# Performance work log

Hardware: AMD Instinct MI355X
Metric: run time of the kernel (lower is better)

Reference implementation:

```python
import jax, jax.numpy as jnp
import numpy as np
from jax import lax

B, C_IN, C_OUT, N, R, K = 16, 64, 64, 32768, 32, 3
GROUPS, GN_EPS = 8, 1e-5


def swish(x):
    return x * jax.nn.sigmoid(x)


def group_norm(x, gamma, beta):
    b, c = x.shape[:2]
    xg = x.reshape(b, GROUPS, -1)
    mu = xg.mean(-1, keepdims=True)
    var = xg.var(-1, keepdims=True)
    xn = ((xg - mu) * lax.rsqrt(var + GN_EPS)).reshape(x.shape)
    shp = (1, c) + (1,) * (x.ndim - 2)
    return xn * gamma.reshape(shp) + beta.reshape(shp)


def conv3d(x, w, b):
    y = lax.conv_general_dilated(x, w, (1, 1, 1), 'SAME',
                                 dimension_numbers=('NCDHW', 'OIDHW', 'NCDHW'))
    return y + b.reshape(1, -1, 1, 1, 1)


def voxelize(features, coords):
    # features [B,C,N], coords [B,3,N] -> vox [B,C,R,R,R], norm_coords [B,3,N] in [0,R-1]
    c = coords - coords.mean(axis=2, keepdims=True)
    scale = jnp.linalg.norm(c, axis=1, keepdims=True).max(axis=2, keepdims=True) * 2.0  # eps=0
    norm = jnp.clip((c / scale + 0.5) * R, 0.0, R - 1)
    vc = jnp.round(norm).astype(jnp.int32)
    idx = (vc[:, 0] * R + vc[:, 1]) * R + vc[:, 2]  # [B,N] flat voxel index

    def per_batch(f, i):  # f [C,N], i [N] -> [C, R^3] scatter-average
        sums = jax.ops.segment_sum(f.T, i, num_segments=R ** 3)  # [R^3, C]
        cnt = jax.ops.segment_sum(jnp.ones(i.shape, f.dtype), i, num_segments=R ** 3)
        return (sums / jnp.maximum(cnt, 1.0)[:, None]).T

    vox = jax.vmap(per_batch)(features, idx).reshape(features.shape[0], features.shape[1], R, R, R)
    return vox, norm


def trilinear_devoxelize(vox, coords):
    # vox [B,C,R,R,R], coords [B,3,N] float in [0,R-1] -> [B,C,N]
    b, c = vox.shape[:2]
    flat = vox.reshape(b, c, R ** 3)
    c0f = jnp.floor(coords)
    f = coords - c0f
    i0 = jnp.clip(c0f.astype(jnp.int32), 0, R - 1)
    i1 = jnp.clip(i0 + 1, 0, R - 1)
    out = jnp.zeros((b, c, coords.shape[2]), vox.dtype)
    for xi, wx in ((i0[:, 0], 1.0 - f[:, 0]), (i1[:, 0], f[:, 0])):
        for yi, wy in ((i0[:, 1], 1.0 - f[:, 1]), (i1[:, 1], f[:, 1])):
            for zi, wz in ((i0[:, 2], 1.0 - f[:, 2]), (i1[:, 2], f[:, 2])):
                idx = (xi * R + yi) * R + zi  # [B,N]
                w = (wx * wy * wz)[:, None, :]
                out = out + jnp.take_along_axis(flat, idx[:, None, :], axis=2) * w
    return out


def setup_inputs():
    key = jax.random.key(0)
    ks = jax.random.split(key, 6)
    s1 = 1.0 / np.sqrt(C_IN * K ** 3)
    s2 = 1.0 / np.sqrt(C_OUT * K ** 3)
    sp = 1.0 / np.sqrt(C_IN)
    return {
        'features': jax.random.normal(ks[0], (B, C_IN, N), jnp.float32),
        'coords': jax.random.normal(ks[1], (B, 3, N), jnp.float32),
        'w1': jax.random.normal(ks[2], (C_OUT, C_IN, K, K, K), jnp.float32) * s1,
        'b1': jnp.zeros((C_OUT,), jnp.float32),
        'g1': jnp.ones((C_OUT,), jnp.float32),
        'be1': jnp.zeros((C_OUT,), jnp.float32),
        'w2': jax.random.normal(ks[3], (C_OUT, C_OUT, K, K, K), jnp.float32) * s2,
        'b2': jnp.zeros((C_OUT,), jnp.float32),
        'g2': jnp.ones((C_OUT,), jnp.float32),
        'be2': jnp.zeros((C_OUT,), jnp.float32),
        'wp': jax.random.normal(ks[4], (C_OUT, C_IN), jnp.float32) * sp,
        'bp': jnp.zeros((C_OUT,), jnp.float32),
        'gp': jnp.ones((C_OUT,), jnp.float32),
        'bep': jnp.zeros((C_OUT,), jnp.float32),
    }


def reference(features, coords, w1, b1, g1, be1, w2, b2, g2, be2, wp, bp, gp, bep):
    coords_sg = lax.stop_gradient(coords)  # torch: coords.detach() inside Voxelization
    vox, norm_coords = voxelize(features, coords_sg)
    h = swish(group_norm(conv3d(vox, w1, b1), g1, be1))
    # Dropout(0.1) is identity in eval mode
    h = swish(group_norm(conv3d(h, w2, b2), g2, be2))
    vpts = trilinear_devoxelize(h, norm_coords)
    pf = swish(group_norm(jnp.einsum('oc,bcn->bon', wp, features) + bp[None, :, None], gp, bep))
    return (vpts + pf, coords)
```

## Files before the change

kernel.cpp:

```cpp
#include <hip/hip_runtime.h>
#include <hip/hip_bf16.h>
#include <math.h>

#define BB   16
#define CCH  64
#define NPT  32768
#define RR   32
#define R3   32768
#define GSZ  262144
#define VOXB 2228224

typedef __attribute__((ext_vector_type(8))) short bfx8;
typedef __attribute__((ext_vector_type(8))) unsigned short usx8;
typedef __attribute__((ext_vector_type(16))) float f32x16;

__device__ __forceinline__ short f2bf(float f) {
    unsigned u = __builtin_bit_cast(unsigned, f);
    u += 0x7fff + ((u >> 16) & 1);
    return (short)(u >> 16);
}
__device__ __forceinline__ float bf2f(unsigned short s) {
    unsigned u = ((unsigned)s) << 16;
    return __builtin_bit_cast(float, u);
}

__device__ __forceinline__ float blockReduceSumF(float v) {
    __shared__ float sm[16];
    #pragma unroll
    for (int o = 32; o > 0; o >>= 1) v += __shfl_down(v, o);
    __syncthreads();
    if ((threadIdx.x & 63) == 0) sm[threadIdx.x >> 6] = v;
    __syncthreads();
    float s = 0.f;
    int nw = blockDim.x >> 6;
    for (int i = 0; i < nw; ++i) s += sm[i];
    return s;
}

__device__ __forceinline__ float blockReduceMaxF(float v) {
    __shared__ float sm[16];
    #pragma unroll
    for (int o = 32; o > 0; o >>= 1) v = fmaxf(v, __shfl_down(v, o));
    __syncthreads();
    if ((threadIdx.x & 63) == 0) sm[threadIdx.x >> 6] = v;
    __syncthreads();
    float s = sm[0];
    int nw = blockDim.x >> 6;
    for (int i = 1; i < nw; ++i) s = fmaxf(s, sm[i]);
    return s;
}

__global__ void k_cstat_sum(const float* __restrict__ coords, float* __restrict__ csum) {
    int b = blockIdx.x >> 3, seg = blockIdx.x & 7;
    const float* cb = coords + (size_t)b * 3 * NPT;
    int n0 = seg << 12;
    float sx = 0.f, sy = 0.f, sz = 0.f;
    for (int n = n0 + threadIdx.x; n < n0 + 4096; n += 256) {
        sx += cb[n]; sy += cb[NPT + n]; sz += cb[2 * NPT + n];
    }
    sx = blockReduceSumF(sx);
    sy = blockReduceSumF(sy);
    sz = blockReduceSumF(sz);
    if (threadIdx.x == 0) {
        atomicAdd(&csum[b * 4 + 0], sx);
        atomicAdd(&csum[b * 4 + 1], sy);
        atomicAdd(&csum[b * 4 + 2], sz);
    }
}

__global__ void k_cstat_max(const float* __restrict__ coords, const float* __restrict__ csum,
                            int* __restrict__ cmax) {
    int b = blockIdx.x >> 3, seg = blockIdx.x & 7;
    const float* cb = coords + (size_t)b * 3 * NPT;
    float mx = csum[b * 4 + 0] * (1.f / NPT);
    float my = csum[b * 4 + 1] * (1.f / NPT);
    float mz = csum[b * 4 + 2] * (1.f / NPT);
    int n0 = seg << 12;
    float mn = 0.f;
    for (int n = n0 + threadIdx.x; n < n0 + 4096; n += 256) {
        float x = cb[n] - mx, y = cb[NPT + n] - my, z = cb[2 * NPT + n] - mz;
        mn = fmaxf(mn, sqrtf(x * x + y * y + z * z));
    }
    mn = blockReduceMaxF(mn);
    if (threadIdx.x == 0) atomicMax(&cmax[b], __float_as_int(mn));
}

__global__ void k_norm_idx(const float* __restrict__ coords, const float* __restrict__ csum,
                           const int* __restrict__ cmax,
                           float* __restrict__ normc, int* __restrict__ vidx,
                           int* __restrict__ hist, float* __restrict__ out2) {
    int t = blockIdx.x * 256 + threadIdx.x;
    int b = t >> 15, n = t & 32767;
    float mx = csum[b * 4 + 0] * (1.f / NPT);
    float my = csum[b * 4 + 1] * (1.f / NPT);
    float mz = csum[b * 4 + 2] * (1.f / NPT);
    float scale = 2.f * __int_as_float(cmax[b]);
    const float* cb = coords + (size_t)b * 3 * NPT;
    float x = cb[n], y = cb[NPT + n], z = cb[2 * NPT + n];
    float nx = fminf(fmaxf(((x - mx) / scale + 0.5f) * 32.f, 0.f), 31.f);
    float ny = fminf(fmaxf(((y - my) / scale + 0.5f) * 32.f, 0.f), 31.f);
    float nz = fminf(fmaxf(((z - mz) / scale + 0.5f) * 32.f, 0.f), 31.f);
    float* nb = normc + (size_t)b * 3 * NPT;
    nb[n] = nx; nb[NPT + n] = ny; nb[2 * NPT + n] = nz;
    int vx = (int)rintf(nx), vy = (int)rintf(ny), vz = (int)rintf(nz);
    int v = (vx * 32 + vy) * 32 + vz;
    vidx[t] = v;
    atomicAdd(&hist[(b << 15) + v], 1);
    float* o2 = out2 + (size_t)b * 3 * NPT;
    o2[n] = x; o2[NPT + n] = y; o2[2 * NPT + n] = z;
}

__global__ __launch_bounds__(1024) void k_prefix(const int* __restrict__ hist,
                                                 int* __restrict__ startB,
                                                 int* __restrict__ base) {
    int b = blockIdx.x;
    int tid = threadIdx.x;
    const int* h = hist + (b << 15);
    int loc[32];
    int s = 0;
    #pragma unroll
    for (int j = 0; j < 32; ++j) { loc[j] = h[tid * 32 + j]; s += loc[j]; }
    __shared__ int sm[1024];
    sm[tid] = s;
    __syncthreads();
    for (int o = 1; o < 1024; o <<= 1) {
        int v = (tid >= o) ? sm[tid - o] : 0;
        __syncthreads();
        sm[tid] += v;
        __syncthreads();
    }
    int run = (tid ? sm[tid - 1] : 0);
    #pragma unroll
    for (int j = 0; j < 32; ++j) {
        int idx = (b << 15) + tid * 32 + j;
        startB[idx] = run;
        base[idx] = run;
        run += loc[j];
    }
}

__global__ __launch_bounds__(256) void k_reorder(const float* __restrict__ feat,
                                                 const int* __restrict__ vidx,
                                                 int* __restrict__ base,
                                                 short* __restrict__ featT) {
    __shared__ float tile[64][65];
    __shared__ int sslot[64];
    int blk = blockIdx.x;
    int b = blk >> 9;
    int n0 = (blk & 511) << 6;
    int tid = threadIdx.x;
    const float* fb = feat + ((size_t)b << 21);
    for (int e = tid; e < 64 * 16; e += 256) {
        int c = e >> 4, n4 = e & 15;
        float4 v4 = *(const float4*)(fb + ((size_t)c << 15) + n0 + n4 * 4);
        tile[c][n4 * 4 + 0] = v4.x; tile[c][n4 * 4 + 1] = v4.y;
        tile[c][n4 * 4 + 2] = v4.z; tile[c][n4 * 4 + 3] = v4.w;
    }
    if (tid < 64) {
        int v = vidx[(b << 15) + n0 + tid];
        sslot[tid] = atomicAdd(&base[(b << 15) + v], 1);
    }
    __syncthreads();
    int p = tid >> 2, q = tid & 3;
    int slot = sslot[p];
    short* dst = featT + (((size_t)((b << 15) + slot)) << 6) + q * 16;
    unsigned pk[8];
    #pragma unroll
    for (int k = 0; k < 8; ++k) {
        unsigned lo16 = (unsigned short)f2bf(tile[q * 16 + 2 * k][p]);
        unsigned hi16 = (unsigned short)f2bf(tile[q * 16 + 2 * k + 1][p]);
        pk[k] = lo16 | (hi16 << 16);
    }
    *(int4*)dst = make_int4(pk[0], pk[1], pk[2], pk[3]);
    *(int4*)(dst + 8) = make_int4(pk[4], pk[5], pk[6], pk[7]);
}

__global__ void k_vox_accum(const short* __restrict__ featT, const int* __restrict__ startB,
                            const int* __restrict__ base, short* __restrict__ vout) {
    int t = blockIdx.x * 256 + threadIdx.x;
    int lane4 = t & 15;
    int v = (t >> 4) & 32767;
    int b = t >> 19;
    int start = startB[(b << 15) + v];
    int end   = base[(b << 15) + v];
    float4 acc = make_float4(0.f, 0.f, 0.f, 0.f);
    const short* fT = featT + (((size_t)b << 15) << 6) + lane4 * 4;
    for (int p = start; p < end; ++p) {
        short4 hv = *(const short4*)(fT + ((size_t)p << 6));
        acc.x += bf2f((unsigned short)hv.x);
        acc.y += bf2f((unsigned short)hv.y);
        acc.z += bf2f((unsigned short)hv.z);
        acc.w += bf2f((unsigned short)hv.w);
    }
    float rc = 1.f / fmaxf((float)(end - start), 1.f);
    short4 pk;
    pk.x = f2bf(acc.x * rc); pk.y = f2bf(acc.y * rc);
    pk.z = f2bf(acc.z * rc); pk.w = f2bf(acc.w * rc);
    *(short4*)(vout + (size_t)b * VOXB + ((size_t)(v >> 5) * 34 + (v & 31) + 1) * 64 + lane4 * 4) = pk;
}

__global__ void k_padzero(short* __restrict__ v) {
    int t = blockIdx.x * 256 + threadIdx.x;
    int q = t & 7, zp = (t >> 3) & 1, xy = (t >> 4) & 1023, b = t >> 14;
    int z = zp ? 33 : 0;
    *(int4*)(v + (size_t)b * VOXB + ((size_t)xy * 34 + z) * 64 + q * 8) = make_int4(0, 0, 0, 0);
}

__global__ void k_wprep(const float* __restrict__ w, short* __restrict__ wT) {
    int e = blockIdx.x * 256 + threadIdx.x;
    int ci = e & 63, co = (e >> 6) & 63, k = e >> 12;
    wT[e] = f2bf(w[(size_t)(co * 64 + ci) * 27 + k]);
}

template<bool FUSE>
__global__ __launch_bounds__(512, 4) void k_conv_mfma(
    const short* __restrict__ vin, const short* __restrict__ wT,
    const float* __restrict__ bias,
    const float* __restrict__ stin, const float* __restrict__ gin,
    const float* __restrict__ bein,
    short* __restrict__ vout, float* __restrict__ st)
{
    __shared__ short lds[36 * 1088];
    __shared__ float sred[8][2];
    int bid = blockIdx.x;
    int xcd = bid & 7, sub = bid >> 3;
    int b = (xcd << 1) | (sub >> 6);
    int tile = sub & 63;
    int x0 = (tile >> 3) << 2, y0 = (tile & 7) << 2;
    int tid = threadIdx.x;
    int wv8 = tid >> 6;
    int cb = wv8 & 1, xl = wv8 >> 1;
    int l = tid & 63, lo = l & 31, hi = l >> 5;
    const short* vb = vin + (size_t)b * VOXB;
    int xo = x0 + xl;
    if (tid < 16) ((float*)sred)[tid] = 0.f;

    f32x16 acc[4];
    #pragma unroll
    for (int j = 0; j < 4; ++j)
        #pragma unroll
        for (int i = 0; i < 16; ++i) acc[j][i] = 0.f;

    #pragma unroll
    for (int h = 0; h < 2; ++h) {
        if (h) __syncthreads();
        for (int e = tid; e < 4896; e += 512) {
            int line = e / 136, r = e - line * 136;
            int z = r >> 2, q = r & 3;
            int xx = line / 6, yy = line - xx * 6;
            int xi = x0 + xx - 1, yi = y0 + yy - 1;
            bool inb = ((unsigned)xi < 32u) && ((unsigned)yi < 32u);
            int4 v = make_int4(0, 0, 0, 0);
            if (inb)
                v = *(const int4*)(vb + ((size_t)(xi * 32 + yi) * 34 + z) * 64 + h * 32 + q * 8);
            if (FUSE) {
                if (inb && z >= 1 && z <= 32) {
                    int ci0 = h * 32 + q * 8, cg = ci0 >> 3;
                    float s = stin[((b << 3) + cg) * 2 + 0];
                    float s2 = stin[((b << 3) + cg) * 2 + 1];
                    float mean = s * (1.f / 262144.f);
                    float rstd = rsqrtf(s2 * (1.f / 262144.f) - mean * mean + 1e-5f);
                    float4 ga = *(const float4*)(gin + ci0);
                    float4 gb = *(const float4*)(gin + ci0 + 4);
                    float4 ba = *(const float4*)(bein + ci0);
                    float4 bb = *(const float4*)(bein + ci0 + 4);
                    float gm[8] = {ga.x, ga.y, ga.z, ga.w, gb.x, gb.y, gb.z, gb.w};
                    float bt[8] = {ba.x, ba.y, ba.z, ba.w, bb.x, bb.y, bb.z, bb.w};
                    unsigned short* hv = (unsigned short*)&v;
                    #pragma unroll
                    for (int i = 0; i < 8; ++i) {
                        float f = bf2f(hv[i]);
                        float g = (f - mean) * rstd * gm[i] + bt[i];
                        float sw = g / (1.f + __expf(-g));
                        hv[i] = (unsigned short)f2bf(sw);
                    }
                }
            }
            int dst = line * 1088 + z * 32 + ((q * 8) ^ ((z & 3) << 3));
            *(int4*)(lds + dst) = v;
        }
        __syncthreads();
        const short* wbase = wT + lo * 64 + h * 32 + hi * 8 + cb * 2048;
        #pragma unroll
        for (int dx = 0; dx < 3; ++dx) {
            const short* ldsx = lds + ((xl + dx) * 6) * 1088;
            #pragma unroll
            for (int dz = 0; dz < 3; ++dz) {
                int zz = lo + dz;
                int swz = (zz & 3) << 3;
                const short* bcol = ldsx + zz * 32;
                #pragma unroll
                for (int s = 0; s < 2; ++s) {
                    int slot = (s * 16 + hi * 8) ^ swz;
                    const short* wt0 = wbase + (dx * 9 + dz) * 4096 + s * 16;
                    bfx8 w0 = *(const bfx8*)(wt0);
                    bfx8 w1 = *(const bfx8*)(wt0 + 3 * 4096);
                    bfx8 w2 = *(const bfx8*)(wt0 + 6 * 4096);
                    #pragma unroll
                    for (int L = 0; L < 6; ++L) {
                        bfx8 bv = *(const bfx8*)(bcol + L * 1088 + slot);
                        if (L <= 3)
                            acc[L] = __builtin_amdgcn_mfma_f32_32x32x16_bf16(w0, bv, acc[L], 0, 0, 0);
                        if (L >= 1 && L <= 4)
                            acc[L-1] = __builtin_amdgcn_mfma_f32_32x32x16_bf16(w1, bv, acc[L-1], 0, 0, 0);
                        if (L >= 2)
                            acc[L-2] = __builtin_amdgcn_mfma_f32_32x32x16_bf16(w2, bv, acc[L-2], 0, 0, 0);
                    }
                }
            }
        }
    }

    float gs[4], gs2[4];
    #pragma unroll
    for (int g = 0; g < 4; ++g) { gs[g] = 0.f; gs2[g] = 0.f; }
    short* ob = vout + (size_t)b * VOXB;
    #pragma unroll
    for (int j = 0; j < 4; ++j) {
        size_t rb = ((size_t)(xo * 32 + y0 + j) * 34 + 1 + lo) * 64;
        #pragma unroll
        for (int q = 0; q < 4; ++q) {
            int co0 = cb * 32 + hi * 4 + q * 8;
            float v0 = acc[j][q * 4 + 0] + bias[co0 + 0];
            float v1 = acc[j][q * 4 + 1] + bias[co0 + 1];
            float v2 = acc[j][q * 4 + 2] + bias[co0 + 2];
            float v3 = acc[j][q * 4 + 3] + bias[co0 + 3];
            gs[q] += v0 + v1 + v2 + v3;
            gs2[q] += v0 * v0 + v1 * v1 + v2 * v2 + v3 * v3;
            short4 pk;
            pk.x = f2bf(v0); pk.y = f2bf(v1); pk.z = f2bf(v2); pk.w = f2bf(v3);
            *(short4*)(ob + rb + co0) = pk;
        }
    }
    #pragma unroll
    for (int q = 0; q < 4; ++q) {
        float s = gs[q], s2 = gs2[q];
        #pragma unroll
        for (int o = 32; o > 0; o >>= 1) { s += __shfl_down(s, o); s2 += __shfl_down(s2, o); }
        if (l == 0) { atomicAdd(&sred[cb * 4 + q][0], s); atomicAdd(&sred[cb * 4 + q][1], s2); }
    }
    __syncthreads();
    if (tid < 8) {
        atomicAdd(&st[((b << 3) + tid) * 2 + 0], sred[tid][0]);
        atomicAdd(&st[((b << 3) + tid) * 2 + 1], sred[tid][1]);
    }
}

__global__ void k_gn_apply_b(short* __restrict__ v, const float* __restrict__ st,
                             const float* __restrict__ gamma, const float* __restrict__ beta) {
    int e = blockIdx.x * 256 + threadIdx.x;
    int cg = e & 7, vx = (e >> 3) & 32767, b = e >> 18;
    float s = st[(b * 8 + cg) * 2 + 0], s2 = st[(b * 8 + cg) * 2 + 1];
    float mean = s * (1.f / 262144.f);
    float var = s2 * (1.f / 262144.f) - mean * mean;
    float rstd = rsqrtf(var + 1e-5f);
    short* p = v + (size_t)b * VOXB + ((size_t)(vx >> 5) * 34 + (vx & 31) + 1) * 64 + cg * 8;
    usx8 hv = *(const usx8*)p;
    usx8 ov;
    #pragma unroll
    for (int i = 0; i < 8; ++i) {
        int co = cg * 8 + i;
        float f = bf2f(hv[i]);
        float g = (f - mean) * rstd * gamma[co] + beta[co];
        float sw = g / (1.f + __expf(-g));
        ov[i] = (unsigned short)f2bf(sw);
    }
    *(usx8*)p = ov;
}

__global__ __launch_bounds__(256) void k_point(const float* __restrict__ feat,
                                               const float* __restrict__ wp,
                                               const float* __restrict__ bp,
                                               short* __restrict__ pbuf,
                                               float* __restrict__ stp) {
    __shared__ float s_f[64][64];
    __shared__ float s_w[64][68];
    __shared__ float sred[8][2];
    int nblk = blockIdx.x * 64;
    int b = blockIdx.y;
    int tid = threadIdx.x;
    if (tid < 16) ((float*)sred)[tid] = 0.f;
    const float* fb = feat + (((size_t)b * CCH) << 15);
    for (int e = tid; e < 64 * 64; e += 256) {
        int c = e >> 6, nn = e & 63;
        s_f[c][nn] = fb[(((size_t)c) << 15) + nblk + nn];
        s_w[nn][c] = wp[e];
    }
    __syncthreads();
    int o0 = (tid >> 4) << 2;
    int n0 = (tid & 15) << 2;
    float acc[4][4] = {{0.f}};
    for (int c = 0; c < 64; ++c) {
        float4 fv = *(const float4*)&s_f[c][n0];
        float4 wv = *(const float4*)&s_w[c][o0];
        float fvv[4] = {fv.x, fv.y, fv.z, fv.w};
        float wvv[4] = {wv.x, wv.y, wv.z, wv.w};
        #pragma unroll
        for (int j = 0; j < 4; ++j)
            #pragma unroll
            for (int i = 0; i < 4; ++i) acc[j][i] += wvv[j] * fvv[i];
    }
    float s = 0.f, s2 = 0.f;
    #pragma unroll
    for (int j = 0; j < 4; ++j) {
        float bb = bp[o0 + j];
        short* op = pbuf + (((size_t)(b * CCH + o0 + j)) << 15) + nblk + n0;
        short4 pk;
        float v0 = acc[j][0] + bb, v1 = acc[j][1] + bb;
        float v2 = acc[j][2] + bb, v3 = acc[j][3] + bb;
        s += v0 + v1 + v2 + v3;
        s2 += v0 * v0 + v1 * v1 + v2 * v2 + v3 * v3;
        pk.x = f2bf(v0); pk.y = f2bf(v1); pk.z = f2bf(v2); pk.w = f2bf(v3);
        *(short4*)op = pk;
    }
    int g = o0 >> 3;
    atomicAdd(&sred[g][0], s);
    atomicAdd(&sred[g][1], s2);
    __syncthreads();
    if (tid < 8) {
        atomicAdd(&stp[(b * 8 + tid) * 2 + 0], sred[tid][0]);
        atomicAdd(&stp[(b * 8 + tid) * 2 + 1], sred[tid][1]);
    }
}

__global__ void k_final(const short* __restrict__ h, const float* __restrict__ normc,
                        const float* __restrict__ stp, const float* __restrict__ gp,
                        const float* __restrict__ bep, const short* __restrict__ pbuf,
                        float* __restrict__ out1) {
    int tid = threadIdx.x;
    int s = tid & 7, pp = tid >> 3;
    int pt = blockIdx.x * 32 + pp;
    int b = pt >> 15, n = pt & 32767;
    const float* nb = normc + (size_t)b * 3 * NPT;
    float nx = nb[n], ny = nb[NPT + n], nz = nb[2 * NPT + n];
    float fxf = floorf(nx), fyf = floorf(ny), fzf = floorf(nz);
    float fx = nx - fxf, fy = ny - fyf, fz = nz - fzf;
    int x0 = (int)fxf; x0 = x0 < 31 ? x0 : 31;
    int y0 = (int)fyf; y0 = y0 < 31 ? y0 : 31;
    int z0 = (int)fzf; z0 = z0 < 31 ? z0 : 31;
    int x1 = x0 + 1 < 31 ? x0 + 1 : 31;
    int y1 = y0 + 1 < 31 ? y0 + 1 : 31;
    int z1 = z0 + 1 < 31 ? z0 + 1 : 31;
    float wx0 = 1.f - fx, wx1 = fx, wy0 = 1.f - fy, wy1 = fy, wz0 = 1.f - fz, wz1 = fz;
    const short* hb = h + (size_t)b * VOXB + s * 8;
    float acc[8];
    #pragma unroll
    for (int i = 0; i < 8; ++i) acc[i] = 0.f;
    #pragma unroll
    for (int cx = 0; cx < 2; ++cx) {
        int xi = cx ? x1 : x0; float wxx = cx ? wx1 : wx0;
        #pragma unroll
        for (int cy = 0; cy < 2; ++cy) {
            int yi = cy ? y1 : y0; float wyy = cy ? wy1 : wy0;
            #pragma unroll
            for (int cz = 0; cz < 2; ++cz) {
                int zi = cz ? z1 : z0; float wzz = cz ? wz1 : wz0;
                float w = wxx * wyy * wzz;
                usx8 hv = *(const usx8*)(hb + ((size_t)(xi * 32 + yi) * 34 + zi + 1) * 64);
                #pragma unroll
                for (int i = 0; i < 8; ++i) acc[i] = fmaf(w, bf2f(hv[i]), acc[i]);
            }
        }
    }
    float ss = stp[(b * 8 + s) * 2 + 0], ss2 = stp[(b * 8 + s) * 2 + 1];
    float mean = ss * (1.f / 262144.f);
    float rstd = rsqrtf(ss2 * (1.f / 262144.f) - mean * mean + 1e-5f);
    const short* pb = pbuf + (((size_t)(b * CCH)) << 15) + n;
    #pragma unroll
    for (int i = 0; i < 8; ++i) {
        int co = s * 8 + i;
        float* op = out1 + (((size_t)(b * CCH + co)) << 15) + n;
        float pv = bf2f((unsigned short)pb[((size_t)co) << 15]);
        float g = (pv - mean) * rstd * gp[co] + bep[co];
        float sw = g / (1.f + __expf(-g));
        *op = acc[i] + sw;
    }
}

extern "C" void kernel_launch(void* const* d_in, const int* in_sizes, int n_in,
                              void* d_out, int out_size, void* d_ws, size_t ws_size,
                              hipStream_t stream) {
    const float* feat   = (const float*)d_in[0];
    const float* coords = (const float*)d_in[1];
    const float* w1  = (const float*)d_in[2];
    const float* b1  = (const float*)d_in[3];
    const float* g1  = (const float*)d_in[4];
    const float* be1 = (const float*)d_in[5];
    const float* w2  = (const float*)d_in[6];
    const float* b2  = (const float*)d_in[7];
    const float* g2  = (const float*)d_in[8];
    const float* be2 = (const float*)d_in[9];
    const float* wp  = (const float*)d_in[10];
    const float* bp  = (const float*)d_in[11];
    const float* gp  = (const float*)d_in[12];
    const float* bep = (const float*)d_in[13];

    float* out1 = (float*)d_out;
    float* out2 = out1 + (size_t)BB * CCH * NPT;

    const size_t reg0Bytes = (size_t)BB * NPT * CCH * 4;
    short* featT    = (short*)d_ws;
    short* voxT_mid = (short*)d_ws;
    short* pbuf     = (short*)d_ws;
    short* voxT_in  = (short*)((char*)d_ws + reg0Bytes);
    char* p = (char*)voxT_in + (size_t)BB * VOXB * 2;
    int*   hist   = (int*)p;  p += (size_t)BB * R3 * 4;
    int*   startB = (int*)p;  p += (size_t)BB * R3 * 4;
    int*   base   = (int*)p;  p += (size_t)BB * R3 * 4;
    float* normc = (float*)p; p += (size_t)BB * 3 * NPT * 4;
    int*   vidx  = (int*)p;   p += (size_t)BB * NPT * 4;
    short* wT1   = (short*)p; p += 110592 * 2;
    short* wT2   = (short*)p; p += 110592 * 2;
    float* st1   = (float*)p; p += 256 * 4;
    float* st2   = (float*)p; p += 256 * 4;
    float* stp   = (float*)p; p += 256 * 4;
    float* csum  = (float*)p; p += 64 * 4;
    int*   cmax  = (int*)p;   p += 16 * 4;

    hipMemsetAsync(hist, 0, (size_t)BB * R3 * 4, stream);
    hipMemsetAsync(st1, 0, (256 * 3 + 64 + 16) * 4, stream);

    k_padzero<<<1024, 256, 0, stream>>>(voxT_in);
    k_cstat_sum<<<128, 256, 0, stream>>>(coords, csum);
    k_cstat_max<<<128, 256, 0, stream>>>(coords, csum, cmax);
    k_norm_idx<<<(BB * NPT) / 256, 256, 0, stream>>>(coords, csum, cmax, normc, vidx, hist, out2);
    k_prefix<<<BB, 1024, 0, stream>>>(hist, startB, base);
    k_reorder<<<(BB * NPT) / 64, 256, 0, stream>>>(feat, vidx, base, featT);
    k_vox_accum<<<(BB * R3 * 16) / 256, 256, 0, stream>>>(featT, startB, base, voxT_in);
    k_wprep<<<432, 256, 0, stream>>>(w1, wT1);
    k_wprep<<<432, 256, 0, stream>>>(w2, wT2);

    k_padzero<<<1024, 256, 0, stream>>>(voxT_mid);

    k_conv_mfma<false><<<1024, 512, 0, stream>>>(voxT_in, wT1, b1,
                                                 nullptr, nullptr, nullptr, voxT_mid, st1);
    k_conv_mfma<true><<<1024, 512, 0, stream>>>(voxT_mid, wT2, b2,
                                                st1, g1, be1, voxT_in, st2);
    k_gn_apply_b<<<(BB * R3 * 8) / 256, 256, 0, stream>>>(voxT_in, st2, g2, be2);

    k_point<<<dim3(NPT / 64, BB), 256, 0, stream>>>(feat, wp, bp, pbuf, stp);

    k_final<<<(BB * NPT) / 32, 256, 0, stream>>>(voxT_in, normc, stp, gp, bep, pbuf, out1);
}
```

Measured before the change: 720.2 us.

## Fuse second GroupNorm+swish into devoxelize gather, stage output stores, tweak conv LDS swizzle

```diff
diff --git a/kernel.cpp b/kernel.cpp
--- a/kernel.cpp
+++ b/kernel.cpp
@@ -22,6 +22,10 @@
 __device__ __forceinline__ float bf2f(unsigned short s) {
     unsigned u = ((unsigned)s) << 16;
     return __builtin_bit_cast(float, u);
+}
+
+__device__ __forceinline__ int fzswz(int z) {
+    return (((z & 3) ^ ((z >> 2) & 3)) << 3);
 }
 
 __device__ __forceinline__ float blockReduceSumF(float v) {
@@ -276,10 +280,11 @@
                     }
                 }
             }
-            int dst = line * 1088 + z * 32 + ((q * 8) ^ ((z & 3) << 3));
+            int dst = line * 1088 + z * 32 + ((q * 8) ^ fzswz(z));
             *(int4*)(lds + dst) = v;
         }
         __syncthreads();
+        __builtin_amdgcn_s_setprio(1);
         const short* wbase = wT + lo * 64 + h * 32 + hi * 8 + cb * 2048;
         #pragma unroll
         for (int dx = 0; dx < 3; ++dx) {
@@ -287,7 +292,7 @@
             #pragma unroll
             for (int dz = 0; dz < 3; ++dz) {
                 int zz = lo + dz;
-                int swz = (zz & 3) << 3;
+                int swz = fzswz(zz);
                 const short* bcol = ldsx + zz * 32;
                 #pragma unroll
                 for (int s = 0; s < 2; ++s) {
@@ -309,6 +314,7 @@
                 }
             }
         }
+        __builtin_amdgcn_s_setprio(0);
     }
 
     float gs[4], gs2[4];
@@ -344,28 +350,6 @@
         atomicAdd(&st[((b << 3) + tid) * 2 + 0], sred[tid][0]);
         atomicAdd(&st[((b << 3) + tid) * 2 + 1], sred[tid][1]);
     }
-}
-
-__global__ void k_gn_apply_b(short* __restrict__ v, const float* __restrict__ st,
-                             const float* __restrict__ gamma, const float* __restrict__ beta) {
-    int e = blockIdx.x * 256 + threadIdx.x;
-    int cg = e & 7, vx = (e >> 3) & 32767, b = e >> 18;
-    float s = st[(b * 8 + cg) * 2 + 0], s2 = st[(b * 8 + cg) * 2 + 1];
-    float mean = s * (1.f / 262144.f);
-    float var = s2 * (1.f / 262144.f) - mean * mean;
-    float rstd = rsqrtf(var + 1e-5f);
-    short* p = v + (size_t)b * VOXB + ((size_t)(vx >> 5) * 34 + (vx & 31) + 1) * 64 + cg * 8;
-    usx8 hv = *(const usx8*)p;
-    usx8 ov;
-    #pragma unroll
-    for (int i = 0; i < 8; ++i) {
-        int co = cg * 8 + i;
-        float f = bf2f(hv[i]);
-        float g = (f - mean) * rstd * gamma[co] + beta[co];
-        float sw = g / (1.f + __expf(-g));
-        ov[i] = (unsigned short)f2bf(sw);
-    }
-    *(usx8*)p = ov;
 }
 
 __global__ __launch_bounds__(256) void k_point(const float* __restrict__ feat,
@@ -423,14 +407,20 @@
     }
 }
 
-__global__ void k_final(const short* __restrict__ h, const float* __restrict__ normc,
-                        const float* __restrict__ stp, const float* __restrict__ gp,
-                        const float* __restrict__ bep, const short* __restrict__ pbuf,
-                        float* __restrict__ out1) {
+__global__ __launch_bounds__(256) void k_final(
+    const short* __restrict__ h, const float* __restrict__ normc,
+    const float* __restrict__ st2, const float* __restrict__ g2v,
+    const float* __restrict__ be2v,
+    const float* __restrict__ stp, const float* __restrict__ gp,
+    const float* __restrict__ bep, const short* __restrict__ pbuf,
+    float* __restrict__ out1) {
+    __shared__ float sm[64][33];
     int tid = threadIdx.x;
     int s = tid & 7, pp = tid >> 3;
-    int pt = blockIdx.x * 32 + pp;
-    int b = pt >> 15, n = pt & 32767;
+    int blk = blockIdx.x;
+    int b = blk >> 10;
+    int n0 = (blk & 1023) << 5;
+    int n = n0 + pp;
     const float* nb = normc + (size_t)b * 3 * NPT;
     float nx = nb[n], ny = nb[NPT + n], nz = nb[2 * NPT + n];
     float fxf = floorf(nx), fyf = floorf(ny), fzf = floorf(nz);
@@ -442,6 +432,18 @@
     int y1 = y0 + 1 < 31 ? y0 + 1 : 31;
     int z1 = z0 + 1 < 31 ? z0 + 1 : 31;
     float wx0 = 1.f - fx, wx1 = fx, wy0 = 1.f - fy, wy1 = fy, wz0 = 1.f - fz, wz1 = fz;
+
+    float s2m = st2[(b * 8 + s) * 2 + 0], s2q = st2[(b * 8 + s) * 2 + 1];
+    float mean2 = s2m * (1.f / 262144.f);
+    float rstd2 = rsqrtf(s2q * (1.f / 262144.f) - mean2 * mean2 + 1e-5f);
+    float scl[8], sft[8];
+    #pragma unroll
+    for (int i = 0; i < 8; ++i) {
+        float gmm = g2v[s * 8 + i];
+        scl[i] = gmm * rstd2;
+        sft[i] = be2v[s * 8 + i] - mean2 * gmm * rstd2;
+    }
+
     const short* hb = h + (size_t)b * VOXB + s * 8;
     float acc[8];
     #pragma unroll
@@ -458,7 +460,11 @@
                 float w = wxx * wyy * wzz;
                 usx8 hv = *(const usx8*)(hb + ((size_t)(xi * 32 + yi) * 34 + zi + 1) * 64);
                 #pragma unroll
-                for (int i = 0; i < 8; ++i) acc[i] = fmaf(w, bf2f(hv[i]), acc[i]);
+                for (int i = 0; i < 8; ++i) {
+                    float g = bf2f(hv[i]) * scl[i] + sft[i];
+                    float sw = g / (1.f + __expf(-g));
+                    acc[i] = fmaf(w, sw, acc[i]);
+                }
             }
         }
     }
@@ -469,12 +475,18 @@
     #pragma unroll
     for (int i = 0; i < 8; ++i) {
         int co = s * 8 + i;
-        float* op = out1 + (((size_t)(b * CCH + co)) << 15) + n;
         float pv = bf2f((unsigned short)pb[((size_t)co) << 15]);
         float g = (pv - mean) * rstd * gp[co] + bep[co];
         float sw = g / (1.f + __expf(-g));
-        *op = acc[i] + sw;
-    }
+        sm[co][pp] = acc[i] + sw;
+    }
+    __syncthreads();
+    int co = tid >> 2, q = (tid & 3) << 3;
+    float r0 = sm[co][q + 0], r1 = sm[co][q + 1], r2 = sm[co][q + 2], r3 = sm[co][q + 3];
+    float r4 = sm[co][q + 4], r5 = sm[co][q + 5], r6 = sm[co][q + 6], r7 = sm[co][q + 7];
+    float* op = out1 + (((size_t)(b * CCH + co)) << 15) + n0 + q;
+    *(float4*)op = make_float4(r0, r1, r2, r3);
+    *(float4*)(op + 4) = make_float4(r4, r5, r6, r7);
 }
 
 extern "C" void kernel_launch(void* const* d_in, const int* in_sizes, int n_in,
@@ -536,9 +548,9 @@
                                                  nullptr, nullptr, nullptr, voxT_mid, st1);
     k_conv_mfma<true><<<1024, 512, 0, stream>>>(voxT_mid, wT2, b2,
                                                 st1, g1, be1, voxT_in, st2);
-    k_gn_apply_b<<<(BB * R3 * 8) / 256, 256, 0, stream>>>(voxT_in, st2, g2, be2);
 
     k_point<<<dim3(NPT / 64, BB), 256, 0, stream>>>(feat, wp, bp, pbuf, stp);
 
-    k_final<<<(BB * NPT) / 32, 256, 0, stream>>>(voxT_in, normc, stp, gp, bep, pbuf, out1);
-}
+    k_final<<<(BB * NPT) / 32, 256, 0, stream>>>(voxT_in, normc, st2, g2, be2,
+                                                 stp, gp, bep, pbuf, out1);
+}
```

After: 742.4 us. 1.03x slower.
